# Optimization experiments

Hardware: AMD Instinct MI355X
Metric: run time of the kernel (lower is better)

## Reference

```python
import jax, jax.numpy as jnp
import numpy as np

HIDDEN = 256
BATCH = 16
SEQ = 8192


def setup_inputs() -> dict:
    key = jax.random.key(0)
    k1, k2 = jax.random.split(key)
    x = jax.random.normal(k1, (BATCH, SEQ, HIDDEN), dtype=jnp.float32)
    # rotor_net parameters: Linear(hidden, hidden) followed by tanh
    W = jax.random.normal(k2, (HIDDEN, HIDDEN), dtype=jnp.float32) / np.sqrt(HIDDEN)
    b = jnp.zeros((HIDDEN,), dtype=jnp.float32)
    return {"x": x, "W": W, "b": b}


def reference(x, W, b):
    # Original torch code loops over subseq_size=10 chunks of the flattened
    # (B*S, H) tokens, applying rotor_net to each chunk and concatenating.
    # rotor_net is row-wise (Linear + tanh), so chunked application is
    # mathematically identical to one batched application over all tokens.
    B, S, H = x.shape
    flat = x.reshape(-1, H)                      # (B*S, H)
    out = jnp.tanh(flat @ W.T + b)               # (B*S, H)
    return out.reshape(B, S, -1)
```

## Files before the change

### kernel.cpp

```cpp
#include <hip/hip_runtime.h>
#include <hip/hip_bf16.h>


#define HIDDEN 256
#define M_TOTAL (16 * 8192)

using bf16x8 = __attribute__((ext_vector_type(8))) __bf16;
using bf16x4 = __attribute__((ext_vector_type(4))) __bf16;
using f32x4  = __attribute__((ext_vector_type(4))) float;

__device__ __forceinline__ bf16x4 cvt4(float4 v) {
    bf16x4 r;
    r[0] = (__bf16)v.x; r[1] = (__bf16)v.y;
    r[2] = (__bf16)v.z; r[3] = (__bf16)v.w;
    return r;
}

__global__ __launch_bounds__(256) void wfrag_kernel(const float* __restrict__ W,
                                                    __bf16* __restrict__ WF) {
    const int gid  = blockIdx.x * 256 + threadIdx.x;
    const int lane = gid & 63;
    const int t    = (gid >> 6) & 3;
    const int c    = (gid >> 8) & 7;
    const int nb   = gid >> 11;
    const int lr = lane & 15, q = lane >> 4;
    const float* src = W + (size_t)(nb * 64 + t * 16 + lr) * HIDDEN + c * 32 + q * 8;
    float4 lo = *(const float4*)src;
    float4 hi = *(const float4*)(src + 4);
    bf16x8 v;
    v[0] = (__bf16)lo.x; v[1] = (__bf16)lo.y; v[2] = (__bf16)lo.z; v[3] = (__bf16)lo.w;
    v[4] = (__bf16)hi.x; v[5] = (__bf16)hi.y; v[6] = (__bf16)hi.z; v[7] = (__bf16)hi.w;
    *(bf16x8*)(WF + (size_t)gid * 8) = v;
}

__global__ __launch_bounds__(256, 4) void rotor_kernel(const float* __restrict__ X,
                                                       const __bf16* __restrict__ WF,
                                                       const float* __restrict__ bias,
                                                       float* __restrict__ Y) {
    __shared__ __align__(16) unsigned char lds_raw[4 * 4352];
    unsigned char* my = lds_raw + (threadIdx.x >> 6) * 4352;
    __bf16* sX = (__bf16*)my;
    float*  sO = (float*)my;

    const int lane = threadIdx.x & 63;
    const int wave = threadIdx.x >> 6;
    const int q = lane >> 4, lr = lane & 15;

    const int g   = blockIdx.x;
    const int x8  = g & 7;
    const int h   = g >> 3;
    const int nbi = h & 3;
    const int mb  = (h >> 2) * 8 + x8;
    const int row0 = mb * 128 + wave * 32;
    const int nbg  = nbi * 64;

    const int xr8 = lane >> 3, qx = (lane & 7) >> 1, lox = lane & 1;
    const float* xsrc = X + (size_t)(row0 + xr8) * HIDDEN + (lane & 7) * 4;
    int woff[4];
#pragma unroll
    for (int j = 0; j < 4; ++j) {
        const int R = j * 8 + xr8;
        woff[j] = (R >> 4) * 512 + (qx * 16 + (R & 15)) * 8 + lox * 4;
    }

    const __bf16* wf = WF + (size_t)nbi * (8 * 4 * 512) + lane * 8;

    float4 xr[4];
    bf16x8 bc[4], bn[4];
#pragma unroll
    for (int j = 0; j < 4; ++j) xr[j] = *(const float4*)(xsrc + (size_t)j * 8 * HIDDEN);
#pragma unroll
    for (int t = 0; t < 4; ++t) bc[t] = *(const bf16x8*)(wf + t * 512);
#pragma unroll
    for (int j = 0; j < 4; ++j) *(bf16x4*)(sX + woff[j]) = cvt4(xr[j]);

    f32x4 acc[2][4];
#pragma unroll
    for (int m = 0; m < 2; ++m)
#pragma unroll
        for (int t = 0; t < 4; ++t)
            acc[m][t] = (f32x4){0.f, 0.f, 0.f, 0.f};

#pragma unroll
    for (int c = 0; c < 8; ++c) {
        if (c < 7) {
#pragma unroll
            for (int j = 0; j < 4; ++j)
                xr[j] = *(const float4*)(xsrc + (size_t)j * 8 * HIDDEN + (c + 1) * 32);
#pragma unroll
            for (int t = 0; t < 4; ++t)
                bn[t] = *(const bf16x8*)(wf + ((c + 1) * 4 + t) * 512);
        }
        const __bf16* ab = sX + (c & 1) * 1024 + lane * 8;
        bf16x8 a0 = *(const bf16x8*)ab;
        bf16x8 a1 = *(const bf16x8*)(ab + 512);

        acc[0][0] = __builtin_amdgcn_mfma_f32_16x16x32_bf16(a0, bc[0], acc[0][0], 0, 0, 0);
        acc[0][1] = __builtin_amdgcn_mfma_f32_16x16x32_bf16(a0, bc[1], acc[0][1], 0, 0, 0);
        acc[0][2] = __builtin_amdgcn_mfma_f32_16x16x32_bf16(a0, bc[2], acc[0][2], 0, 0, 0);
        acc[0][3] = __builtin_amdgcn_mfma_f32_16x16x32_bf16(a0, bc[3], acc[0][3], 0, 0, 0);
        acc[1][0] = __builtin_amdgcn_mfma_f32_16x16x32_bf16(a1, bc[0], acc[1][0], 0, 0, 0);
        acc[1][1] = __builtin_amdgcn_mfma_f32_16x16x32_bf16(a1, bc[1], acc[1][1], 0, 0, 0);
        acc[1][2] = __builtin_amdgcn_mfma_f32_16x16x32_bf16(a1, bc[2], acc[1][2], 0, 0, 0);
        acc[1][3] = __builtin_amdgcn_mfma_f32_16x16x32_bf16(a1, bc[3], acc[1][3], 0, 0, 0);

        if (c < 7) {
#pragma unroll
            for (int j = 0; j < 4; ++j)
                *(bf16x4*)(sX + ((c + 1) & 1) * 1024 + woff[j]) = cvt4(xr[j]);
#pragma unroll
            for (int t = 0; t < 4; ++t) bc[t] = bn[t];
        }
    }

    float bv[4];
#pragma unroll
    for (int t = 0; t < 4; ++t) bv[t] = bias[nbg + t * 16 + lr];

    float* yb = Y + (size_t)row0 * HIDDEN + nbg;
#pragma unroll
    for (int m = 0; m < 2; ++m) {
#pragma unroll
        for (int t = 0; t < 4; ++t)
#pragma unroll
            for (int r = 0; r < 4; ++r) {
                float z = acc[m][t][r] + bv[t];
                z = fminf(fmaxf(z, -10.f), 10.f);
                const float e2 = __expf(2.0f * z);
                sO[(q * 4 + r) * 68 + t * 16 + lr] = __fdividef(e2 - 1.0f, e2 + 1.0f);
            }
#pragma unroll
        for (int j = 0; j < 4; ++j) {
            float4 v = *(const float4*)(sO + (j * 4 + q) * 68 + lr * 4);
            *(float4*)(yb + (size_t)(m * 16 + j * 4 + q) * HIDDEN + lr * 4) = v;
        }
    }
}

extern "C" void kernel_launch(void* const* d_in, const int* in_sizes, int n_in,
                              void* d_out, int out_size, void* d_ws, size_t ws_size,
                              hipStream_t stream) {
    const float* X    = (const float*)d_in[0];
    const float* W    = (const float*)d_in[1];
    const float* bias = (const float*)d_in[2];
    float* Y          = (float*)d_out;
    __bf16* WF        = (__bf16*)d_ws;

    wfrag_kernel<<<dim3(32), dim3(256), 0, stream>>>(W, WF);
    rotor_kernel<<<dim3((M_TOTAL / 128) * (HIDDEN / 64)), dim3(256), 0, stream>>>(X, WF, bias, Y);
}
```

Baseline: 260.0 us.

## Make persistent blocks hold W in registers and share X tiles across waves

```diff
diff --git a/kernel.cpp b/kernel.cpp
--- a/kernel.cpp
+++ b/kernel.cpp
@@ -4,6 +4,8 @@
 
 #define HIDDEN 256
 #define M_TOTAL (16 * 8192)
+#define NBLK 512
+#define CHUNKS_PER_BLK ((M_TOTAL / 32) / NBLK)
 
 using bf16x8 = __attribute__((ext_vector_type(8))) __bf16;
 using bf16x4 = __attribute__((ext_vector_type(4))) __bf16;
@@ -33,107 +35,112 @@
     *(bf16x8*)(WF + (size_t)gid * 8) = v;
 }
 
-__global__ __launch_bounds__(256, 4) void rotor_kernel(const float* __restrict__ X,
+__global__ __launch_bounds__(256, 2) void rotor_kernel(const float* __restrict__ X,
                                                        const __bf16* __restrict__ WF,
                                                        const float* __restrict__ bias,
                                                        float* __restrict__ Y) {
-    __shared__ __align__(16) unsigned char lds_raw[4 * 4352];
-    unsigned char* my = lds_raw + (threadIdx.x >> 6) * 4352;
-    __bf16* sX = (__bf16*)my;
-    float*  sO = (float*)my;
+    __shared__ __align__(16) unsigned char lds_raw[2 * 16384 + 4 * 4352];
+    __bf16* sXb = (__bf16*)lds_raw;
+    float*  sO  = (float*)(lds_raw + 32768 + (threadIdx.x >> 6) * 4352);
 
-    const int lane = threadIdx.x & 63;
-    const int wave = threadIdx.x >> 6;
-    const int q = lane >> 4, lr = lane & 15;
+    const int tid  = threadIdx.x;
+    const int lane = tid & 63;
+    const int wave = tid >> 6;
+    const int lr = lane & 15, q = lane >> 4;
 
-    const int g   = blockIdx.x;
-    const int x8  = g & 7;
-    const int h   = g >> 3;
-    const int nbi = h & 3;
-    const int mb  = (h >> 2) * 8 + x8;
-    const int row0 = mb * 128 + wave * 32;
-    const int nbg  = nbi * 64;
+    const int xrow = tid >> 3;
+    const int xc   = tid & 7;
+    int woff[8];
+#pragma unroll
+    for (int j = 0; j < 8; ++j)
+        woff[j] = j * 1024 + (xrow >> 4) * 512 + ((xc >> 1) * 16 + (xrow & 15)) * 8 + (xc & 1) * 4;
 
-    const int xr8 = lane >> 3, qx = (lane & 7) >> 1, lox = lane & 1;
-    const float* xsrc = X + (size_t)(row0 + xr8) * HIDDEN + (lane & 7) * 4;
-    int woff[4];
+    const size_t blk_row0 = (size_t)blockIdx.x * (CHUNKS_PER_BLK * 32);
+    const float* xbase = X + (blk_row0 + xrow) * HIDDEN + xc * 4;
+
+    float4 xr[8];
 #pragma unroll
-    for (int j = 0; j < 4; ++j) {
-        const int R = j * 8 + xr8;
-        woff[j] = (R >> 4) * 512 + (qx * 16 + (R & 15)) * 8 + lox * 4;
-    }
+    for (int j = 0; j < 8; ++j) xr[j] = *(const float4*)(xbase + j * 32);
 
-    const __bf16* wf = WF + (size_t)nbi * (8 * 4 * 512) + lane * 8;
-
-    float4 xr[4];
-    bf16x8 bc[4], bn[4];
+    const __bf16* wf = WF + (size_t)wave * (8 * 4 * 512) + lane * 8;
+    bf16x8 bW[8][4];
 #pragma unroll
-    for (int j = 0; j < 4; ++j) xr[j] = *(const float4*)(xsrc + (size_t)j * 8 * HIDDEN);
-#pragma unroll
-    for (int t = 0; t < 4; ++t) bc[t] = *(const bf16x8*)(wf + t * 512);
-#pragma unroll
-    for (int j = 0; j < 4; ++j) *(bf16x4*)(sX + woff[j]) = cvt4(xr[j]);
-
-    f32x4 acc[2][4];
-#pragma unroll
-    for (int m = 0; m < 2; ++m)
+    for (int c = 0; c < 8; ++c)
 #pragma unroll
         for (int t = 0; t < 4; ++t)
-            acc[m][t] = (f32x4){0.f, 0.f, 0.f, 0.f};
-
-#pragma unroll
-    for (int c = 0; c < 8; ++c) {
-        if (c < 7) {
-#pragma unroll
-            for (int j = 0; j < 4; ++j)
-                xr[j] = *(const float4*)(xsrc + (size_t)j * 8 * HIDDEN + (c + 1) * 32);
-#pragma unroll
-            for (int t = 0; t < 4; ++t)
-                bn[t] = *(const bf16x8*)(wf + ((c + 1) * 4 + t) * 512);
-        }
-        const __bf16* ab = sX + (c & 1) * 1024 + lane * 8;
-        bf16x8 a0 = *(const bf16x8*)ab;
-        bf16x8 a1 = *(const bf16x8*)(ab + 512);
-
-        acc[0][0] = __builtin_amdgcn_mfma_f32_16x16x32_bf16(a0, bc[0], acc[0][0], 0, 0, 0);
-        acc[0][1] = __builtin_amdgcn_mfma_f32_16x16x32_bf16(a0, bc[1], acc[0][1], 0, 0, 0);
-        acc[0][2] = __builtin_amdgcn_mfma_f32_16x16x32_bf16(a0, bc[2], acc[0][2], 0, 0, 0);
-        acc[0][3] = __builtin_amdgcn_mfma_f32_16x16x32_bf16(a0, bc[3], acc[0][3], 0, 0, 0);
-        acc[1][0] = __builtin_amdgcn_mfma_f32_16x16x32_bf16(a1, bc[0], acc[1][0], 0, 0, 0);
-        acc[1][1] = __builtin_amdgcn_mfma_f32_16x16x32_bf16(a1, bc[1], acc[1][1], 0, 0, 0);
-        acc[1][2] = __builtin_amdgcn_mfma_f32_16x16x32_bf16(a1, bc[2], acc[1][2], 0, 0, 0);
-        acc[1][3] = __builtin_amdgcn_mfma_f32_16x16x32_bf16(a1, bc[3], acc[1][3], 0, 0, 0);
-
-        if (c < 7) {
-#pragma unroll
-            for (int j = 0; j < 4; ++j)
-                *(bf16x4*)(sX + ((c + 1) & 1) * 1024 + woff[j]) = cvt4(xr[j]);
-#pragma unroll
-            for (int t = 0; t < 4; ++t) bc[t] = bn[t];
-        }
-    }
+            bW[c][t] = *(const bf16x8*)(wf + (c * 4 + t) * 512);
 
     float bv[4];
 #pragma unroll
-    for (int t = 0; t < 4; ++t) bv[t] = bias[nbg + t * 16 + lr];
+    for (int t = 0; t < 4; ++t) bv[t] = bias[wave * 64 + t * 16 + lr];
 
-    float* yb = Y + (size_t)row0 * HIDDEN + nbg;
 #pragma unroll
-    for (int m = 0; m < 2; ++m) {
+    for (int j = 0; j < 8; ++j) *(bf16x4*)(sXb + woff[j]) = cvt4(xr[j]);
+    asm volatile("s_waitcnt lgkmcnt(0)" ::: "memory");
+    __builtin_amdgcn_s_barrier();
+    asm volatile("" ::: "memory");
+
+#pragma unroll 1
+    for (int it = 0; it < CHUNKS_PER_BLK; ++it) {
+        const int cur = it & 1;
+
+        if (it + 1 < CHUNKS_PER_BLK) {
+            const float* xs = xbase + (size_t)(it + 1) * 32 * HIDDEN;
 #pragma unroll
-        for (int t = 0; t < 4; ++t)
+            for (int j = 0; j < 8; ++j) xr[j] = *(const float4*)(xs + j * 32);
+        }
+
+        f32x4 acc[2][4];
 #pragma unroll
-            for (int r = 0; r < 4; ++r) {
-                float z = acc[m][t][r] + bv[t];
-                z = fminf(fmaxf(z, -10.f), 10.f);
-                const float e2 = __expf(2.0f * z);
-                sO[(q * 4 + r) * 68 + t * 16 + lr] = __fdividef(e2 - 1.0f, e2 + 1.0f);
+        for (int m = 0; m < 2; ++m)
+#pragma unroll
+            for (int t = 0; t < 4; ++t)
+                acc[m][t] = (f32x4){0.f, 0.f, 0.f, 0.f};
+
+        const __bf16* sX = sXb + cur * 8192;
+#pragma unroll
+        for (int c = 0; c < 8; ++c) {
+            const __bf16* ab = sX + c * 1024 + lane * 8;
+            bf16x8 a0 = *(const bf16x8*)ab;
+            bf16x8 a1 = *(const bf16x8*)(ab + 512);
+            acc[0][0] = __builtin_amdgcn_mfma_f32_16x16x32_bf16(a0, bW[c][0], acc[0][0], 0, 0, 0);
+            acc[0][1] = __builtin_amdgcn_mfma_f32_16x16x32_bf16(a0, bW[c][1], acc[0][1], 0, 0, 0);
+            acc[0][2] = __builtin_amdgcn_mfma_f32_16x16x32_bf16(a0, bW[c][2], acc[0][2], 0, 0, 0);
+            acc[0][3] = __builtin_amdgcn_mfma_f32_16x16x32_bf16(a0, bW[c][3], acc[0][3], 0, 0, 0);
+            acc[1][0] = __builtin_amdgcn_mfma_f32_16x16x32_bf16(a1, bW[c][0], acc[1][0], 0, 0, 0);
+            acc[1][1] = __builtin_amdgcn_mfma_f32_16x16x32_bf16(a1, bW[c][1], acc[1][1], 0, 0, 0);
+            acc[1][2] = __builtin_amdgcn_mfma_f32_16x16x32_bf16(a1, bW[c][2], acc[1][2], 0, 0, 0);
+            acc[1][3] = __builtin_amdgcn_mfma_f32_16x16x32_bf16(a1, bW[c][3], acc[1][3], 0, 0, 0);
+        }
+
+        float* yb = Y + (blk_row0 + (size_t)it * 32) * HIDDEN + wave * 64;
+#pragma unroll
+        for (int m = 0; m < 2; ++m) {
+#pragma unroll
+            for (int t = 0; t < 4; ++t)
+#pragma unroll
+                for (int r = 0; r < 4; ++r) {
+                    float z = acc[m][t][r] + bv[t];
+                    z = fminf(fmaxf(z, -10.f), 10.f);
+                    const float e2 = __expf(2.0f * z);
+                    sO[(q * 4 + r) * 68 + t * 16 + lr] = __fdividef(e2 - 1.0f, e2 + 1.0f);
+                }
+#pragma unroll
+            for (int j = 0; j < 4; ++j) {
+                f32x4 v = *(const f32x4*)(sO + (j * 4 + q) * 68 + lr * 4);
+                __builtin_nontemporal_store(v,
+                    (f32x4*)(yb + (size_t)(m * 16 + j * 4 + q) * HIDDEN + lr * 4));
             }
+        }
+
+        if (it + 1 < CHUNKS_PER_BLK) {
+            __bf16* sW = sXb + (cur ^ 1) * 8192;
 #pragma unroll
-        for (int j = 0; j < 4; ++j) {
-            float4 v = *(const float4*)(sO + (j * 4 + q) * 68 + lr * 4);
-            *(float4*)(yb + (size_t)(m * 16 + j * 4 + q) * HIDDEN + lr * 4) = v;
+            for (int j = 0; j < 8; ++j) *(bf16x4*)(sW + woff[j]) = cvt4(xr[j]);
         }
+        asm volatile("s_waitcnt lgkmcnt(0)" ::: "memory");
+        __builtin_amdgcn_s_barrier();
+        asm volatile("" ::: "memory");
     }
 }
 
@@ -147,5 +154,5 @@
     __bf16* WF        = (__bf16*)d_ws;
 
     wfrag_kernel<<<dim3(32), dim3(256), 0, stream>>>(W, WF);
-    rotor_kernel<<<dim3((M_TOTAL / 128) * (HIDDEN / 64)), dim3(256), 0, stream>>>(X, WF, bias, Y);
+    rotor_kernel<<<dim3(NBLK), dim3(256), 0, stream>>>(X, WF, bias, Y);
 }
```

Result: faster. 246.8 us (-5.1%).
